# Kernel optimization log

Measured on AMD Instinct MI355X. Metric: run time of the kernel, lower is better.

The kernel has to match this reference:

```python
import jax, jax.numpy as jnp
import numpy as np

NUM_FIELDS = 39
VOCAB_PER_FIELD = 1000
EMB = 64
HEADS = 2
LAYERS = 3
BATCH = 16384
FLAT = NUM_FIELDS * EMB  # 2496


def _mhsa(x, Wq, Wk, Wv, Wr):
    # x: [B, n, D]; no scaling (scaling=False in source)
    B, n, D = x.shape
    dh = D // HEADS
    q = (x @ Wq).reshape(B, n, HEADS, dh)
    k = (x @ Wk).reshape(B, n, HEADS, dh)
    v = (x @ Wv).reshape(B, n, HEADS, dh)
    scores = jnp.einsum('bihd,bjhd->bhij', q, k)
    attn = jax.nn.softmax(scores, axis=-1)
    out = jnp.einsum('bhij,bjhd->bihd', attn, v).reshape(B, n, D)
    out = out + x @ Wr  # residual projection (use_res=True)
    return jax.nn.relu(out)


def setup_inputs() -> dict:
    key = jax.random.key(0)
    ks = jax.random.split(key, 12)
    X = jax.random.randint(ks[0], (BATCH, NUM_FIELDS), 0, VOCAB_PER_FIELD, dtype=jnp.int64 if jax.config.jax_enable_x64 else jnp.int32)
    emb_table = jax.random.normal(ks[1], (NUM_FIELDS * VOCAB_PER_FIELD, EMB), jnp.float32) * 0.05
    WQ = jax.random.normal(ks[2], (LAYERS, EMB, EMB), jnp.float32) * 0.05
    WK = jax.random.normal(ks[3], (LAYERS, EMB, EMB), jnp.float32) * 0.05
    WV = jax.random.normal(ks[4], (LAYERS, EMB, EMB), jnp.float32) * 0.05
    WR = jax.random.normal(ks[5], (LAYERS, EMB, EMB), jnp.float32) * 0.05
    W1 = jax.random.normal(ks[6], (FLAT, 512), jnp.float32) * 0.02
    b1 = jnp.zeros((512,), jnp.float32)
    W2 = jax.random.normal(ks[7], (512, 256), jnp.float32) * 0.02
    b2 = jnp.zeros((256,), jnp.float32)
    W3 = jax.random.normal(ks[8], (256, 1), jnp.float32) * 0.02
    b3 = jnp.zeros((1,), jnp.float32)
    Wlin = jax.random.normal(ks[9], (FLAT, 1), jnp.float32) * 0.02
    return {"X": X, "emb_table": emb_table, "WQ": WQ, "WK": WK, "WV": WV,
            "WR": WR, "W1": W1, "b1": b1, "W2": W2, "b2": b2, "W3": W3,
            "b3": b3, "Wlin": Wlin}


def reference(X, emb_table, WQ, WK, WV, WR, W1, b1, W2, b2, W3, b3, Wlin):
    offsets = jnp.arange(NUM_FIELDS, dtype=X.dtype) * VOCAB_PER_FIELD
    embed_x = emb_table[X + offsets[None, :]]  # [B, n, D]
    att = embed_x
    for i in range(LAYERS):
        att = _mhsa(att, WQ[i], WK[i], WV[i], WR[i])
    B = att.shape[0]
    att_output = jax.nn.relu(att.reshape(B, FLAT) @ Wlin)  # [B,1]
    # MLP: relu follows every Dense, including final 1-unit layer; dropout inactive
    h = embed_x.reshape(B, FLAT)
    h = jax.nn.relu(h @ W1 + b1)
    h = jax.nn.relu(h @ W2 + b2)
    dnn_output = jax.nn.relu(h @ W3 + b3)  # [B,1]
    return jax.nn.sigmoid(att_output + dnn_output)
```

## Files before the change

### kernel.cpp

```cpp
#include <hip/hip_runtime.h>
#include <hip/hip_bf16.h>


#define NF     39
#define EMB    64
#define NLAYER 3
#define VOCAB  1000
#define FLAT   2496
#define H1     512
#define H2     256

typedef __attribute__((ext_vector_type(8))) short  short8;
typedef __attribute__((ext_vector_type(4))) float  floatx4;

__device__ __forceinline__ short8 ld8s(const unsigned short* p) {
    return *(const short8*)p;
}
__device__ __forceinline__ float b2f(unsigned short h) {
    union { unsigned u; float f; } x; x.u = ((unsigned)h) << 16; return x.f;
}
__device__ __forceinline__ unsigned short f2b(float f) {
    union { float f; unsigned u; } x; x.f = f;
    unsigned u = x.u;
    return (unsigned short)((u + 0x7fffu + ((u >> 16) & 1u)) >> 16);
}
__device__ __forceinline__ unsigned cvt_pk(float a, float b) {
#if defined(__gfx950__)
    unsigned r;
    asm("v_cvt_pk_bf16_f32 %0, %1, %2" : "=v"(r) : "v"(a), "v"(b));
    return r;
#else
    return (unsigned)f2b(a) | ((unsigned)f2b(b) << 16);
#endif
}
__device__ __forceinline__ short8 pk8(unsigned a, unsigned b, unsigned c, unsigned d) {
    union { unsigned u[4]; short8 s; } x;
    x.u[0] = a; x.u[1] = b; x.u[2] = c; x.u[3] = d;
    return x.s;
}

__global__ void attw_t(const float* __restrict__ WQ, const float* __restrict__ WK,
                       const float* __restrict__ WV, const float* __restrict__ WR,
                       unsigned short* __restrict__ wqt, unsigned short* __restrict__ wkt,
                       unsigned short* __restrict__ wvt, unsigned short* __restrict__ wrt)
{
    int idx = blockIdx.x * 256 + threadIdx.x;
    if (idx >= 4 * 3 * 4096) return;
    int mat = idx / 12288;
    int rem = idx % 12288;
    int l   = rem / 4096;
    int ok  = rem % 4096;
    int o = ok >> 6, k = ok & 63;
    const float*    src = (mat == 0) ? WQ : (mat == 1) ? WK : (mat == 2) ? WV : WR;
    unsigned short* dst = (mat == 0) ? wqt : (mat == 1) ? wkt : (mat == 2) ? wvt : wrt;
    dst[l * 4096 + o * 64 + k] = f2b(src[l * 4096 + k * 64 + o]);
}

__global__ void w1pack(const float* __restrict__ W1, unsigned short* __restrict__ w1p)
{
    int t = blockIdx.x * 256 + threadIdx.x;
    int lane = t & 63, grp = t >> 6;
    int ot = grp / 78, kk = grp % 78;
    int q = lane >> 4, n = ot * 16 + (lane & 15);
    int kb = kk * 32 + q * 8;
    unsigned short* dst = w1p + grp * 512 + lane * 8;
    #pragma unroll
    for (int j = 0; j < 8; ++j)
        dst[j] = f2b(W1[(kb + j) * 512 + n]);
}

__global__ void w2pack(const float* __restrict__ W2, unsigned short* __restrict__ w2p)
{
    int t = blockIdx.x * 256 + threadIdx.x;
    int lane = t & 63, grp = t >> 6;
    int ot = grp / 16, kk = grp % 16;
    int q = lane >> 4, n = ot * 16 + (lane & 15);
    int kb = kk * 32 + q * 8;
    unsigned short* dst = w2p + grp * 512 + lane * 8;
    #pragma unroll
    for (int j = 0; j < 8; ++j)
        dst[j] = f2b(W2[(kb + j) * 256 + n]);
}

__global__ void __launch_bounds__(128) attn_kernel(
    const int* __restrict__ X,
    const float* __restrict__ embf,
    const unsigned short* __restrict__ wqt,
    const unsigned short* __restrict__ wkt,
    const unsigned short* __restrict__ wvt,
    const unsigned short* __restrict__ wrt,
    const float* __restrict__ wlinf,
    float* __restrict__ att_out)
{
    __shared__ unsigned short xss[48 * 72];
    __shared__ float red[2];

    const int tid  = threadIdx.x;
    const int wid  = tid >> 6;
    const int lane = tid & 63;
    const int h    = wid;
    const int quad = lane >> 4;
    const int l16  = lane & 15;
    const int samp = blockIdx.x;

    {
        const int tq = lane >> 4;
        const int cp = (lane & 15) * 2;
        const int col = h * 32 + cp;
        const int* xrow = X + samp * NF;
        #pragma unroll
        for (int t0 = 0; t0 < 48; t0 += 4) {
            int t = t0 + tq;
            unsigned pk = 0;
            if (t < NF) {
                int row = xrow[t] + t * VOCAB;
                const float2 v = *(const float2*)&embf[row * EMB + col];
                pk = cvt_pk(v.x, v.y);
            }
            *(unsigned*)&xss[t * 72 + col] = pk;
        }
    }
    __syncthreads();

    const int wro = (h * 32 + l16) * 64 + quad * 8;
    const unsigned short* wqp = wqt + wro;
    const unsigned short* wkp = wkt + wro;
    const unsigned short* wvq = wvt + wro;
    const unsigned short* wrp = wrt + wro;
    float m2[4];
    #pragma unroll
    for (int r = 0; r < 4; ++r)
        m2[r] = (32 + quad * 4 + r < NF) ? 1.f : 0.f;

    for (int layer = 0; layer < NLAYER; ++layer) {
        short8 xf[3][2];
        #pragma unroll
        for (int tt = 0; tt < 3; ++tt)
            #pragma unroll
            for (int kk = 0; kk < 2; ++kk)
                xf[tt][kk] = ld8s(&xss[(tt * 16 + l16) * 72 + kk * 32 + quad * 8]);

        __syncthreads();

        unsigned qw[2][3][2], kw[2][3][2];
        #pragma unroll
        for (int mat = 0; mat < 2; ++mat) {
            const unsigned short* wt = mat ? wkp : wqp;
            #pragma unroll
            for (int ot = 0; ot < 2; ++ot) {
                short8 w0 = ld8s(wt + ot * 1024);
                short8 w1 = ld8s(wt + ot * 1024 + 32);
                #pragma unroll
                for (int tt = 0; tt < 3; ++tt) {
                    floatx4 c = {0.f, 0.f, 0.f, 0.f};
                    c = __builtin_amdgcn_mfma_f32_16x16x32_bf16(w0, xf[tt][0], c, 0, 0, 0);
                    c = __builtin_amdgcn_mfma_f32_16x16x32_bf16(w1, xf[tt][1], c, 0, 0, 0);
                    if (mat == 0) {
                        qw[ot][tt][0] = cvt_pk(c[0], c[1]);
                        qw[ot][tt][1] = cvt_pk(c[2], c[3]);
                    } else {
                        kw[ot][tt][0] = cvt_pk(c[0], c[1]);
                        kw[ot][tt][1] = cvt_pk(c[2], c[3]);
                    }
                }
            }
        }

        floatx4 O[2][3];
        #pragma unroll
        for (int dt = 0; dt < 2; ++dt) {
            short8 w0 = ld8s(wrp + dt * 1024);
            short8 w1 = ld8s(wrp + dt * 1024 + 32);
            #pragma unroll
            for (int it = 0; it < 3; ++it) {
                floatx4 c = {0.f, 0.f, 0.f, 0.f};
                c = __builtin_amdgcn_mfma_f32_16x16x32_bf16(w0, xf[it][0], c, 0, 0, 0);
                c = __builtin_amdgcn_mfma_f32_16x16x32_bf16(w1, xf[it][1], c, 0, 0, 0);
                O[dt][it] = c;
            }
        }

        floatx4 ST[3][3];
        #pragma unroll
        for (int jt = 0; jt < 3; ++jt) {
            short8 a = pk8(kw[0][jt][0], kw[0][jt][1], kw[1][jt][0], kw[1][jt][1]);
            #pragma unroll
            for (int it = 0; it < 3; ++it) {
                short8 b = pk8(qw[0][it][0], qw[0][it][1], qw[1][it][0], qw[1][it][1]);
                floatx4 z = {0.f, 0.f, 0.f, 0.f};
                ST[jt][it] = __builtin_amdgcn_mfma_f32_16x16x32_bf16(a, b, z, 0, 0, 0);
            }
        }

        unsigned vw[3][2][2];
        #pragma unroll
        for (int nt = 0; nt < 2; ++nt) {
            short8 w0 = ld8s(wvq + nt * 1024);
            short8 w1 = ld8s(wvq + nt * 1024 + 32);
            #pragma unroll
            for (int mt = 0; mt < 3; ++mt) {
                floatx4 c = {0.f, 0.f, 0.f, 0.f};
                c = __builtin_amdgcn_mfma_f32_16x16x32_bf16(xf[mt][0], w0, c, 0, 0, 0);
                c = __builtin_amdgcn_mfma_f32_16x16x32_bf16(xf[mt][1], w1, c, 0, 0, 0);
                vw[mt][nt][0] = cvt_pk(c[0], c[1]);
                vw[mt][nt][1] = cvt_pk(c[2], c[3]);
            }
        }

        unsigned pw[3][3][2];
        #pragma unroll
        for (int it = 0; it < 3; ++it) {
            float p[3][4];
            float sum = 0.f;
            #pragma unroll
            for (int jt = 0; jt < 3; ++jt)
                #pragma unroll
                for (int r = 0; r < 4; ++r) {
                    float e = __expf(ST[jt][it][r]);
                    if (jt == 2) e *= m2[r];
                    p[jt][r] = e;
                    sum += e;
                }
            sum += __shfl_xor(sum, 16, 64);
            sum += __shfl_xor(sum, 32, 64);
            float inv = 1.0f / sum;
            #pragma unroll
            for (int jt = 0; jt < 3; ++jt) {
                pw[jt][it][0] = cvt_pk(p[jt][0] * inv, p[jt][1] * inv);
                pw[jt][it][1] = cvt_pk(p[jt][2] * inv, p[jt][3] * inv);
            }
        }

        #pragma unroll
        for (int dt = 0; dt < 2; ++dt) {
            short8 a01 = pk8(vw[0][dt][0], vw[0][dt][1], vw[1][dt][0], vw[1][dt][1]);
            short8 a2  = pk8(vw[2][dt][0], vw[2][dt][1], 0u, 0u);
            #pragma unroll
            for (int it = 0; it < 3; ++it) {
                short8 b01 = pk8(pw[0][it][0], pw[0][it][1], pw[1][it][0], pw[1][it][1]);
                short8 b2  = pk8(pw[2][it][0], pw[2][it][1], 0u, 0u);
                O[dt][it] = __builtin_amdgcn_mfma_f32_16x16x32_bf16(a01, b01, O[dt][it], 0, 0, 0);
                O[dt][it] = __builtin_amdgcn_mfma_f32_16x16x32_bf16(a2,  b2,  O[dt][it], 0, 0, 0);
            }
        }

        #pragma unroll
        for (int dt = 0; dt < 2; ++dt)
            #pragma unroll
            for (int it = 0; it < 3; ++it) {
                uint2 w;
                w.x = cvt_pk(fmaxf(O[dt][it][0], 0.f), fmaxf(O[dt][it][1], 0.f));
                w.y = cvt_pk(fmaxf(O[dt][it][2], 0.f), fmaxf(O[dt][it][3], 0.f));
                *(uint2*)&xss[(it * 16 + l16) * 72 + h * 32 + dt * 16 + quad * 4] = w;
            }

        __syncthreads();

        wqp += 4096; wkp += 4096; wvq += 4096; wrp += 4096;
    }

    {
        float acc = 0.f;
        const int c = lane & 31, tp = lane >> 5;
        const int col = h * 32 + c;
        for (int t0 = 0; t0 < 40; t0 += 2) {
            int t = t0 + tp;
            if (t < NF)
                acc += b2f(xss[t * 72 + col]) * wlinf[t * EMB + col];
        }
        #pragma unroll
        for (int off = 1; off < 64; off <<= 1)
            acc += __shfl_xor(acc, off, 64);
        if (lane == 0) red[wid] = acc;
        __syncthreads();
        if (tid == 0)
            att_out[samp] = fmaxf(red[0] + red[1], 0.f);
    }
}

__global__ void __launch_bounds__(256) dnn_kernel(
    const int* __restrict__ X,
    const float* __restrict__ embf,
    const unsigned short* __restrict__ w1p,
    const float* __restrict__ b1v,
    const unsigned short* __restrict__ w2p,
    const float* __restrict__ b2v,
    const float* __restrict__ w3v,
    const float* __restrict__ b3v,
    const float* __restrict__ att_in,
    float* __restrict__ out)
{
    __shared__ unsigned short ea[2][32 * 72];
    __shared__ unsigned short h1s[32 * 520];
    unsigned short* h2s = h1s;

    const int tid  = threadIdx.x;
    const int wid  = tid >> 6, lane = tid & 63, quad = lane >> 4, l16 = lane & 15;
    const int S0   = blockIdx.x * 32;

    floatx4 C1[2][8];
    #pragma unroll
    for (int mt = 0; mt < 2; ++mt)
        #pragma unroll
        for (int nt = 0; nt < 8; ++nt)
            C1[mt][nt] = (floatx4){0.f, 0.f, 0.f, 0.f};

    const int gs = tid >> 3;
    const int gg = tid & 7;

    {
        int row = X[(S0 + gs) * NF + 0];
        const float4* src = (const float4*)&embf[row * EMB + gg * 8];
        float4 v0 = src[0], v1 = src[1];
        uint4 u;
        u.x = cvt_pk(v0.x, v0.y); u.y = cvt_pk(v0.z, v0.w);
        u.z = cvt_pk(v1.x, v1.y); u.w = cvt_pk(v1.z, v1.w);
        *(uint4*)&ea[0][gs * 72 + gg * 8] = u;
    }
    __syncthreads();

    for (int f = 0; f < NF; ++f) {
        if (f < NF - 1) {
            int row = X[(S0 + gs) * NF + f + 1] + (f + 1) * VOCAB;
            const float4* src = (const float4*)&embf[row * EMB + gg * 8];
            float4 v0 = src[0], v1 = src[1];
            uint4 u;
            u.x = cvt_pk(v0.x, v0.y); u.y = cvt_pk(v0.z, v0.w);
            u.z = cvt_pk(v1.x, v1.y); u.w = cvt_pk(v1.z, v1.w);
            *(uint4*)&ea[(f + 1) & 1][gs * 72 + gg * 8] = u;
        }
        const unsigned short* eac = ea[f & 1];
        short8 a[2][2];
        #pragma unroll
        for (int mt = 0; mt < 2; ++mt) {
            a[mt][0] = ld8s(&eac[(mt * 16 + l16) * 72 + quad * 8]);
            a[mt][1] = ld8s(&eac[(mt * 16 + l16) * 72 + 32 + quad * 8]);
        }
        #pragma unroll
        for (int nt = 0; nt < 8; ++nt) {
            const unsigned short* bp = w1p + (((wid * 8 + nt) * 78 + f * 2) * 64 + lane) * 8;
            short8 b0 = ld8s(bp);
            short8 b1 = ld8s(bp + 512);
            #pragma unroll
            for (int mt = 0; mt < 2; ++mt) {
                C1[mt][nt] = __builtin_amdgcn_mfma_f32_16x16x32_bf16(a[mt][0], b0, C1[mt][nt], 0, 0, 0);
                C1[mt][nt] = __builtin_amdgcn_mfma_f32_16x16x32_bf16(a[mt][1], b1, C1[mt][nt], 0, 0, 0);
            }
        }
        __syncthreads();
    }

    #pragma unroll
    for (int nt = 0; nt < 8; ++nt) {
        float bb = b1v[wid * 128 + nt * 16 + l16];
        #pragma unroll
        for (int mt = 0; mt < 2; ++mt) {
            #pragma unroll
            for (int r = 0; r < 4; ++r) {
                float v = fmaxf(C1[mt][nt][r] + bb, 0.f);
                h1s[(mt * 16 + quad * 4 + r) * 520 + wid * 128 + nt * 16 + l16] = f2b(v);
            }
        }
    }
    __syncthreads();

    floatx4 C2[2][4];
    #pragma unroll
    for (int mt = 0; mt < 2; ++mt)
        #pragma unroll
        for (int nt = 0; nt < 4; ++nt)
            C2[mt][nt] = (floatx4){0.f, 0.f, 0.f, 0.f};

    #pragma unroll 4
    for (int kk = 0; kk < 16; ++kk) {
        short8 a0 = ld8s(&h1s[(l16) * 520 + kk * 32 + quad * 8]);
        short8 a1 = ld8s(&h1s[(16 + l16) * 520 + kk * 32 + quad * 8]);
        #pragma unroll
        for (int nt = 0; nt < 4; ++nt) {
            short8 b = ld8s(w2p + (((wid * 4 + nt) * 16 + kk) * 64 + lane) * 8);
            C2[0][nt] = __builtin_amdgcn_mfma_f32_16x16x32_bf16(a0, b, C2[0][nt], 0, 0, 0);
            C2[1][nt] = __builtin_amdgcn_mfma_f32_16x16x32_bf16(a1, b, C2[1][nt], 0, 0, 0);
        }
    }
    __syncthreads();

    #pragma unroll
    for (int nt = 0; nt < 4; ++nt) {
        float bb = b2v[wid * 64 + nt * 16 + l16];
        #pragma unroll
        for (int mt = 0; mt < 2; ++mt)
            #pragma unroll
            for (int r = 0; r < 4; ++r)
                h2s[(mt * 16 + quad * 4 + r) * 264 + wid * 64 + nt * 16 + l16] =
                    f2b(fmaxf(C2[mt][nt][r] + bb, 0.f));
    }
    __syncthreads();

    {
        int s = tid >> 3, part = tid & 7;
        float acc = 0.f;
        #pragma unroll 8
        for (int j = 0; j < 32; ++j) {
            int jj = part * 32 + j;
            acc += b2f(h2s[s * 264 + jj]) * w3v[jj];
        }
        acc += __shfl_xor(acc, 1, 64);
        acc += __shfl_xor(acc, 2, 64);
        acc += __shfl_xor(acc, 4, 64);
        if (part == 0) {
            float dnn = fmaxf(acc + b3v[0], 0.f);
            float v = dnn + att_in[S0 + s];
            out[S0 + s] = 1.f / (1.f + __expf(-v));
        }
    }
}

extern "C" void kernel_launch(void* const* d_in, const int* in_sizes, int n_in,
                              void* d_out, int out_size, void* d_ws, size_t ws_size,
                              hipStream_t stream)
{
    (void)in_sizes; (void)n_in; (void)out_size; (void)ws_size;

    const int*   X    = (const int*)d_in[0];
    const float* emb  = (const float*)d_in[1];
    const float* WQ   = (const float*)d_in[2];
    const float* WK   = (const float*)d_in[3];
    const float* WV   = (const float*)d_in[4];
    const float* WR   = (const float*)d_in[5];
    const float* W1   = (const float*)d_in[6];
    const float* b1   = (const float*)d_in[7];
    const float* W2   = (const float*)d_in[8];
    const float* b2   = (const float*)d_in[9];
    const float* W3   = (const float*)d_in[10];
    const float* b3   = (const float*)d_in[11];
    const float* Wlin = (const float*)d_in[12];

    char* ws = (char*)d_ws;
    float*          att_logit = (float*)ws;
    unsigned short* wqt = (unsigned short*)(ws + 65536);
    unsigned short* wkt = wqt + 3 * 4096;
    unsigned short* wvt = wkt + 3 * 4096;
    unsigned short* wrt = wvt + 3 * 4096;
    unsigned short* w1p = wrt + 3 * 4096;
    unsigned short* w2p = w1p + 2496 * 512;

    attw_t<<<192, 256, 0, stream>>>(WQ, WK, WV, WR, wqt, wkt, wvt, wrt);
    w1pack<<<624, 256, 0, stream>>>(W1, w1p);
    w2pack<<<64, 256, 0, stream>>>(W2, w2p);
    attn_kernel<<<16384, 128, 0, stream>>>(X, emb, wqt, wkt, wvt, wrt, Wlin, att_logit);
    dnn_kernel<<<512, 256, 0, stream>>>(X, emb, w1p, b1, w2p, b2, W3, b3, att_logit,
                                        (float*)d_out);
}
```

Baseline: 378.4 us.

## Process two samples per attention block to reuse weight fragments

The attention kernel now handles two samples per 128-thread block, halving the grid. Each Q/K/V/R weight fragment loaded from global memory is reused across both samples' MFMAs, and block launch and barrier overhead is amortized over two samples. In exchange, register pressure roughly doubles (two sets of Q/K/V/O fragments) and shared memory doubles, which could reduce occupancy or cause spills.

```diff
diff --git a/kernel.cpp b/kernel.cpp
--- a/kernel.cpp
+++ b/kernel.cpp
@@ -92,8 +92,8 @@
     const float* __restrict__ wlinf,
     float* __restrict__ att_out)
 {
-    __shared__ unsigned short xss[48 * 72];
-    __shared__ float red[2];
+    __shared__ unsigned short xss[2][48 * 72];
+    __shared__ float red[2][2];
 
     const int tid  = threadIdx.x;
     const int wid  = tid >> 6;
@@ -101,23 +101,26 @@
     const int h    = wid;
     const int quad = lane >> 4;
     const int l16  = lane & 15;
-    const int samp = blockIdx.x;
+    const int samp0 = blockIdx.x * 2;
 
     {
         const int tq = lane >> 4;
         const int cp = (lane & 15) * 2;
         const int col = h * 32 + cp;
-        const int* xrow = X + samp * NF;
-        #pragma unroll
-        for (int t0 = 0; t0 < 48; t0 += 4) {
-            int t = t0 + tq;
-            unsigned pk = 0;
-            if (t < NF) {
-                int row = xrow[t] + t * VOCAB;
-                const float2 v = *(const float2*)&embf[row * EMB + col];
-                pk = cvt_pk(v.x, v.y);
-            }
-            *(unsigned*)&xss[t * 72 + col] = pk;
+        #pragma unroll
+        for (int s = 0; s < 2; ++s) {
+            const int* xrow = X + (samp0 + s) * NF;
+            #pragma unroll
+            for (int t0 = 0; t0 < 48; t0 += 4) {
+                int t = t0 + tq;
+                unsigned pk = 0;
+                if (t < NF) {
+                    int row = xrow[t] + t * VOCAB;
+                    const float2 v = *(const float2*)&embf[row * EMB + col];
+                    pk = cvt_pk(v.x, v.y);
+                }
+                *(unsigned*)&xss[s][t * 72 + col] = pk;
+            }
         }
     }
     __syncthreads();
@@ -133,16 +136,18 @@
         m2[r] = (32 + quad * 4 + r < NF) ? 1.f : 0.f;
 
     for (int layer = 0; layer < NLAYER; ++layer) {
-        short8 xf[3][2];
-        #pragma unroll
-        for (int tt = 0; tt < 3; ++tt)
-            #pragma unroll
-            for (int kk = 0; kk < 2; ++kk)
-                xf[tt][kk] = ld8s(&xss[(tt * 16 + l16) * 72 + kk * 32 + quad * 8]);
+        short8 xf[2][3][2];
+        #pragma unroll
+        for (int s = 0; s < 2; ++s)
+            #pragma unroll
+            for (int tt = 0; tt < 3; ++tt)
+                #pragma unroll
+                for (int kk = 0; kk < 2; ++kk)
+                    xf[s][tt][kk] = ld8s(&xss[s][(tt * 16 + l16) * 72 + kk * 32 + quad * 8]);
 
         __syncthreads();
 
-        unsigned qw[2][3][2], kw[2][3][2];
+        unsigned qw[2][2][3][2], kw[2][2][3][2];
         #pragma unroll
         for (int mat = 0; mat < 2; ++mat) {
             const unsigned short* wt = mat ? wkp : wqp;
@@ -151,108 +156,120 @@
                 short8 w0 = ld8s(wt + ot * 1024);
                 short8 w1 = ld8s(wt + ot * 1024 + 32);
                 #pragma unroll
-                for (int tt = 0; tt < 3; ++tt) {
-                    floatx4 c = {0.f, 0.f, 0.f, 0.f};
-                    c = __builtin_amdgcn_mfma_f32_16x16x32_bf16(w0, xf[tt][0], c, 0, 0, 0);
-                    c = __builtin_amdgcn_mfma_f32_16x16x32_bf16(w1, xf[tt][1], c, 0, 0, 0);
-                    if (mat == 0) {
-                        qw[ot][tt][0] = cvt_pk(c[0], c[1]);
-                        qw[ot][tt][1] = cvt_pk(c[2], c[3]);
-                    } else {
-                        kw[ot][tt][0] = cvt_pk(c[0], c[1]);
-                        kw[ot][tt][1] = cvt_pk(c[2], c[3]);
+                for (int s = 0; s < 2; ++s)
+                    #pragma unroll
+                    for (int tt = 0; tt < 3; ++tt) {
+                        floatx4 c = {0.f, 0.f, 0.f, 0.f};
+                        c = __builtin_amdgcn_mfma_f32_16x16x32_bf16(w0, xf[s][tt][0], c, 0, 0, 0);
+                        c = __builtin_amdgcn_mfma_f32_16x16x32_bf16(w1, xf[s][tt][1], c, 0, 0, 0);
+                        if (mat == 0) {
+                            qw[s][ot][tt][0] = cvt_pk(c[0], c[1]);
+                            qw[s][ot][tt][1] = cvt_pk(c[2], c[3]);
+                        } else {
+                            kw[s][ot][tt][0] = cvt_pk(c[0], c[1]);
+                            kw[s][ot][tt][1] = cvt_pk(c[2], c[3]);
+                        }
                     }
-                }
-            }
-        }
-
-        floatx4 O[2][3];
+            }
+        }
+
+        floatx4 O[2][2][3];
         #pragma unroll
         for (int dt = 0; dt < 2; ++dt) {
             short8 w0 = ld8s(wrp + dt * 1024);
             short8 w1 = ld8s(wrp + dt * 1024 + 32);
             #pragma unroll
-            for (int it = 0; it < 3; ++it) {
-                floatx4 c = {0.f, 0.f, 0.f, 0.f};
-                c = __builtin_amdgcn_mfma_f32_16x16x32_bf16(w0, xf[it][0], c, 0, 0, 0);
-                c = __builtin_amdgcn_mfma_f32_16x16x32_bf16(w1, xf[it][1], c, 0, 0, 0);
-                O[dt][it] = c;
-            }
-        }
-
-        floatx4 ST[3][3];
-        #pragma unroll
-        for (int jt = 0; jt < 3; ++jt) {
-            short8 a = pk8(kw[0][jt][0], kw[0][jt][1], kw[1][jt][0], kw[1][jt][1]);
-            #pragma unroll
-            for (int it = 0; it < 3; ++it) {
-                short8 b = pk8(qw[0][it][0], qw[0][it][1], qw[1][it][0], qw[1][it][1]);
-                floatx4 z = {0.f, 0.f, 0.f, 0.f};
-                ST[jt][it] = __builtin_amdgcn_mfma_f32_16x16x32_bf16(a, b, z, 0, 0, 0);
-            }
-        }
-
-        unsigned vw[3][2][2];
+            for (int s = 0; s < 2; ++s)
+                #pragma unroll
+                for (int it = 0; it < 3; ++it) {
+                    floatx4 c = {0.f, 0.f, 0.f, 0.f};
+                    c = __builtin_amdgcn_mfma_f32_16x16x32_bf16(w0, xf[s][it][0], c, 0, 0, 0);
+                    c = __builtin_amdgcn_mfma_f32_16x16x32_bf16(w1, xf[s][it][1], c, 0, 0, 0);
+                    O[s][dt][it] = c;
+                }
+        }
+
+        unsigned vw[2][3][2][2];
         #pragma unroll
         for (int nt = 0; nt < 2; ++nt) {
             short8 w0 = ld8s(wvq + nt * 1024);
             short8 w1 = ld8s(wvq + nt * 1024 + 32);
             #pragma unroll
-            for (int mt = 0; mt < 3; ++mt) {
-                floatx4 c = {0.f, 0.f, 0.f, 0.f};
-                c = __builtin_amdgcn_mfma_f32_16x16x32_bf16(xf[mt][0], w0, c, 0, 0, 0);
-                c = __builtin_amdgcn_mfma_f32_16x16x32_bf16(xf[mt][1], w1, c, 0, 0, 0);
-                vw[mt][nt][0] = cvt_pk(c[0], c[1]);
-                vw[mt][nt][1] = cvt_pk(c[2], c[3]);
-            }
-        }
-
-        unsigned pw[3][3][2];
-        #pragma unroll
-        for (int it = 0; it < 3; ++it) {
-            float p[3][4];
-            float sum = 0.f;
-            #pragma unroll
-            for (int jt = 0; jt < 3; ++jt)
-                #pragma unroll
-                for (int r = 0; r < 4; ++r) {
-                    float e = __expf(ST[jt][it][r]);
-                    if (jt == 2) e *= m2[r];
-                    p[jt][r] = e;
-                    sum += e;
-                }
-            sum += __shfl_xor(sum, 16, 64);
-            sum += __shfl_xor(sum, 32, 64);
-            float inv = 1.0f / sum;
+            for (int s = 0; s < 2; ++s)
+                #pragma unroll
+                for (int mt = 0; mt < 3; ++mt) {
+                    floatx4 c = {0.f, 0.f, 0.f, 0.f};
+                    c = __builtin_amdgcn_mfma_f32_16x16x32_bf16(xf[s][mt][0], w0, c, 0, 0, 0);
+                    c = __builtin_amdgcn_mfma_f32_16x16x32_bf16(xf[s][mt][1], w1, c, 0, 0, 0);
+                    vw[s][mt][nt][0] = cvt_pk(c[0], c[1]);
+                    vw[s][mt][nt][1] = cvt_pk(c[2], c[3]);
+                }
+        }
+
+        unsigned pw[2][3][3][2];
+        #pragma unroll
+        for (int s = 0; s < 2; ++s) {
+            floatx4 ST[3][3];
             #pragma unroll
             for (int jt = 0; jt < 3; ++jt) {
-                pw[jt][it][0] = cvt_pk(p[jt][0] * inv, p[jt][1] * inv);
-                pw[jt][it][1] = cvt_pk(p[jt][2] * inv, p[jt][3] * inv);
-            }
-        }
-
-        #pragma unroll
-        for (int dt = 0; dt < 2; ++dt) {
-            short8 a01 = pk8(vw[0][dt][0], vw[0][dt][1], vw[1][dt][0], vw[1][dt][1]);
-            short8 a2  = pk8(vw[2][dt][0], vw[2][dt][1], 0u, 0u);
+                short8 a = pk8(kw[s][0][jt][0], kw[s][0][jt][1], kw[s][1][jt][0], kw[s][1][jt][1]);
+                #pragma unroll
+                for (int it = 0; it < 3; ++it) {
+                    short8 b = pk8(qw[s][0][it][0], qw[s][0][it][1], qw[s][1][it][0], qw[s][1][it][1]);
+                    floatx4 z = {0.f, 0.f, 0.f, 0.f};
+                    ST[jt][it] = __builtin_amdgcn_mfma_f32_16x16x32_bf16(a, b, z, 0, 0, 0);
+                }
+            }
             #pragma unroll
             for (int it = 0; it < 3; ++it) {
-                short8 b01 = pk8(pw[0][it][0], pw[0][it][1], pw[1][it][0], pw[1][it][1]);
-                short8 b2  = pk8(pw[2][it][0], pw[2][it][1], 0u, 0u);
-                O[dt][it] = __builtin_amdgcn_mfma_f32_16x16x32_bf16(a01, b01, O[dt][it], 0, 0, 0);
-                O[dt][it] = __builtin_amdgcn_mfma_f32_16x16x32_bf16(a2,  b2,  O[dt][it], 0, 0, 0);
-            }
-        }
-
-        #pragma unroll
-        for (int dt = 0; dt < 2; ++dt)
-            #pragma unroll
-            for (int it = 0; it < 3; ++it) {
-                uint2 w;
-                w.x = cvt_pk(fmaxf(O[dt][it][0], 0.f), fmaxf(O[dt][it][1], 0.f));
-                w.y = cvt_pk(fmaxf(O[dt][it][2], 0.f), fmaxf(O[dt][it][3], 0.f));
-                *(uint2*)&xss[(it * 16 + l16) * 72 + h * 32 + dt * 16 + quad * 4] = w;
-            }
+                float p[3][4];
+                float sum = 0.f;
+                #pragma unroll
+                for (int jt = 0; jt < 3; ++jt)
+                    #pragma unroll
+                    for (int r = 0; r < 4; ++r) {
+                        float e = __expf(ST[jt][it][r]);
+                        if (jt == 2) e *= m2[r];
+                        p[jt][r] = e;
+                        sum += e;
+                    }
+                sum += __shfl_xor(sum, 16, 64);
+                sum += __shfl_xor(sum, 32, 64);
+                float inv = 1.0f / sum;
+                #pragma unroll
+                for (int jt = 0; jt < 3; ++jt) {
+                    pw[s][jt][it][0] = cvt_pk(p[jt][0] * inv, p[jt][1] * inv);
+                    pw[s][jt][it][1] = cvt_pk(p[jt][2] * inv, p[jt][3] * inv);
+                }
+            }
+        }
+
+        #pragma unroll
+        for (int s = 0; s < 2; ++s)
+            #pragma unroll
+            for (int dt = 0; dt < 2; ++dt) {
+                short8 a01 = pk8(vw[s][0][dt][0], vw[s][0][dt][1], vw[s][1][dt][0], vw[s][1][dt][1]);
+                short8 a2  = pk8(vw[s][2][dt][0], vw[s][2][dt][1], 0u, 0u);
+                #pragma unroll
+                for (int it = 0; it < 3; ++it) {
+                    short8 b01 = pk8(pw[s][0][it][0], pw[s][0][it][1], pw[s][1][it][0], pw[s][1][it][1]);
+                    short8 b2  = pk8(pw[s][2][it][0], pw[s][2][it][1], 0u, 0u);
+                    O[s][dt][it] = __builtin_amdgcn_mfma_f32_16x16x32_bf16(a01, b01, O[s][dt][it], 0, 0, 0);
+                    O[s][dt][it] = __builtin_amdgcn_mfma_f32_16x16x32_bf16(a2,  b2,  O[s][dt][it], 0, 0, 0);
+                }
+            }
+
+        #pragma unroll
+        for (int s = 0; s < 2; ++s)
+            #pragma unroll
+            for (int dt = 0; dt < 2; ++dt)
+                #pragma unroll
+                for (int it = 0; it < 3; ++it) {
+                    uint2 w;
+                    w.x = cvt_pk(fmaxf(O[s][dt][it][0], 0.f), fmaxf(O[s][dt][it][1], 0.f));
+                    w.y = cvt_pk(fmaxf(O[s][dt][it][2], 0.f), fmaxf(O[s][dt][it][3], 0.f));
+                    *(uint2*)&xss[s][(it * 16 + l16) * 72 + h * 32 + dt * 16 + quad * 4] = w;
+                }
 
         __syncthreads();
 
@@ -260,21 +277,26 @@
     }
 
     {
-        float acc = 0.f;
         const int c = lane & 31, tp = lane >> 5;
         const int col = h * 32 + c;
-        for (int t0 = 0; t0 < 40; t0 += 2) {
-            int t = t0 + tp;
-            if (t < NF)
-                acc += b2f(xss[t * 72 + col]) * wlinf[t * EMB + col];
-        }
-        #pragma unroll
-        for (int off = 1; off < 64; off <<= 1)
-            acc += __shfl_xor(acc, off, 64);
-        if (lane == 0) red[wid] = acc;
+        #pragma unroll
+        for (int s = 0; s < 2; ++s) {
+            float acc = 0.f;
+            for (int t0 = 0; t0 < 40; t0 += 2) {
+                int t = t0 + tp;
+                if (t < NF)
+                    acc += b2f(xss[s][t * 72 + col]) * wlinf[t * EMB + col];
+            }
+            #pragma unroll
+            for (int off = 1; off < 64; off <<= 1)
+                acc += __shfl_xor(acc, off, 64);
+            if (lane == 0) red[s][wid] = acc;
+        }
         __syncthreads();
-        if (tid == 0)
-            att_out[samp] = fmaxf(red[0] + red[1], 0.f);
+        if (tid == 0) {
+            att_out[samp0]     = fmaxf(red[0][0] + red[0][1], 0.f);
+            att_out[samp0 + 1] = fmaxf(red[1][0] + red[1][1], 0.f);
+        }
     }
 }
 
@@ -447,7 +469,7 @@
     attw_t<<<192, 256, 0, stream>>>(WQ, WK, WV, WR, wqt, wkt, wvt, wrt);
     w1pack<<<624, 256, 0, stream>>>(W1, w1p);
     w2pack<<<64, 256, 0, stream>>>(W2, w2p);
-    attn_kernel<<<16384, 128, 0, stream>>>(X, emb, wqt, wkt, wvt, wrt, Wlin, att_logit);
+    attn_kernel<<<8192, 128, 0, stream>>>(X, emb, wqt, wkt, wvt, wrt, Wlin, att_logit);
     dnn_kernel<<<512, 256, 0, stream>>>(X, emb, w1p, b1, w2p, b2, W3, b3, att_logit,
                                         (float*)d_out);
 }
```

Measured after the change: 362.8 us. 1.04x faster.

## Run one sample per wavefront with register-resident activations, dropping LDS round trips

Applied to the files above, without the earlier changes.

The attention kernel now gives each wavefront a whole sample covering both heads, with four samples per 256-thread block, instead of two wavefronts per sample, one per head. Activations stay in registers between layers as packed bf16 MFMA operands. To make this work, the weight transpose permutes the K index so the MFMA output layout matches the next layer's input layout. This removes shared-memory staging, block barriers and the cross-wave reduction, but raises register pressure and doubles per-wave MFMA work.

```diff
diff --git a/kernel.cpp b/kernel.cpp
--- a/kernel.cpp
+++ b/kernel.cpp
@@ -19,6 +19,8 @@
 __device__ __forceinline__ float b2f(unsigned short h) {
     union { unsigned u; float f; } x; x.u = ((unsigned)h) << 16; return x.f;
 }
+__device__ __forceinline__ float b2f_lo(unsigned w) { return b2f((unsigned short)(w & 0xffffu)); }
+__device__ __forceinline__ float b2f_hi(unsigned w) { return b2f((unsigned short)(w >> 16)); }
 __device__ __forceinline__ unsigned short f2b(float f) {
     union { float f; unsigned u; } x; x.f = f;
     unsigned u = x.u;
@@ -50,10 +52,12 @@
     int rem = idx % 12288;
     int l   = rem / 4096;
     int ok  = rem % 4096;
-    int o = ok >> 6, k = ok & 63;
+    int o = ok >> 6, pos = ok & 63;
+    int kk = pos >> 5, q = (pos >> 3) & 3, e = pos & 7;
+    int k = kk * 32 + (e >> 2) * 16 + q * 4 + (e & 3);
     const float*    src = (mat == 0) ? WQ : (mat == 1) ? WK : (mat == 2) ? WV : WR;
     unsigned short* dst = (mat == 0) ? wqt : (mat == 1) ? wkt : (mat == 2) ? wvt : wrt;
-    dst[l * 4096 + o * 64 + k] = f2b(src[l * 4096 + k * 64 + o]);
+    dst[l * 4096 + o * 64 + pos] = f2b(src[l * 4096 + k * 64 + o]);
 }
 
 __global__ void w1pack(const float* __restrict__ W1, unsigned short* __restrict__ w1p)
@@ -82,7 +86,7 @@
         dst[j] = f2b(W2[(kb + j) * 256 + n]);
 }
 
-__global__ void __launch_bounds__(128) attn_kernel(
+__global__ void __launch_bounds__(256) attn_kernel(
     const int* __restrict__ X,
     const float* __restrict__ embf,
     const unsigned short* __restrict__ wqt,
@@ -92,190 +96,199 @@
     const float* __restrict__ wlinf,
     float* __restrict__ att_out)
 {
-    __shared__ unsigned short xss[48 * 72];
-    __shared__ float red[2];
-
     const int tid  = threadIdx.x;
     const int wid  = tid >> 6;
     const int lane = tid & 63;
-    const int h    = wid;
     const int quad = lane >> 4;
     const int l16  = lane & 15;
-    const int samp = blockIdx.x;
-
+    const int samp = blockIdx.x * 4 + wid;
+
+    unsigned xiw[3][2][4];
     {
-        const int tq = lane >> 4;
-        const int cp = (lane & 15) * 2;
-        const int col = h * 32 + cp;
         const int* xrow = X + samp * NF;
         #pragma unroll
-        for (int t0 = 0; t0 < 48; t0 += 4) {
-            int t = t0 + tq;
-            unsigned pk = 0;
-            if (t < NF) {
-                int row = xrow[t] + t * VOCAB;
-                const float2 v = *(const float2*)&embf[row * EMB + col];
-                pk = cvt_pk(v.x, v.y);
-            }
-            *(unsigned*)&xss[t * 72 + col] = pk;
-        }
-    }
-    __syncthreads();
-
-    const int wro = (h * 32 + l16) * 64 + quad * 8;
-    const unsigned short* wqp = wqt + wro;
-    const unsigned short* wkp = wkt + wro;
-    const unsigned short* wvq = wvt + wro;
-    const unsigned short* wrp = wrt + wro;
+        for (int tt = 0; tt < 3; ++tt) {
+            const int tok = tt * 16 + l16;
+            if (tok < NF) {
+                const int row = xrow[tok] + tok * VOCAB;
+                const float* er = embf + row * EMB;
+                #pragma unroll
+                for (int kk = 0; kk < 2; ++kk) {
+                    const float4 lo = *(const float4*)(er + kk * 32 + quad * 4);
+                    const float4 hi = *(const float4*)(er + kk * 32 + 16 + quad * 4);
+                    xiw[tt][kk][0] = cvt_pk(lo.x, lo.y);
+                    xiw[tt][kk][1] = cvt_pk(lo.z, lo.w);
+                    xiw[tt][kk][2] = cvt_pk(hi.x, hi.y);
+                    xiw[tt][kk][3] = cvt_pk(hi.z, hi.w);
+                }
+            } else {
+                #pragma unroll
+                for (int kk = 0; kk < 2; ++kk)
+                    #pragma unroll
+                    for (int w = 0; w < 4; ++w)
+                        xiw[tt][kk][w] = 0u;
+            }
+        }
+    }
+
+    const int wro_l = l16 * 64 + quad * 8;
+    const unsigned short* wq = wqt + wro_l;
+    const unsigned short* wk = wkt + wro_l;
+    const unsigned short* wv = wvt + wro_l;
+    const unsigned short* wr = wrt + wro_l;
     float m2[4];
     #pragma unroll
     for (int r = 0; r < 4; ++r)
         m2[r] = (32 + quad * 4 + r < NF) ? 1.f : 0.f;
 
+    #define XF(tt,kk) pk8(xiw[tt][kk][0], xiw[tt][kk][1], xiw[tt][kk][2], xiw[tt][kk][3])
+
     for (int layer = 0; layer < NLAYER; ++layer) {
-        short8 xf[3][2];
-        #pragma unroll
-        for (int tt = 0; tt < 3; ++tt)
-            #pragma unroll
-            for (int kk = 0; kk < 2; ++kk)
-                xf[tt][kk] = ld8s(&xss[(tt * 16 + l16) * 72 + kk * 32 + quad * 8]);
-
-        __syncthreads();
-
-        unsigned qw[2][3][2], kw[2][3][2];
-        #pragma unroll
-        for (int mat = 0; mat < 2; ++mat) {
-            const unsigned short* wt = mat ? wkp : wqp;
-            #pragma unroll
-            for (int ot = 0; ot < 2; ++ot) {
-                short8 w0 = ld8s(wt + ot * 1024);
-                short8 w1 = ld8s(wt + ot * 1024 + 32);
-                #pragma unroll
-                for (int tt = 0; tt < 3; ++tt) {
-                    floatx4 c = {0.f, 0.f, 0.f, 0.f};
-                    c = __builtin_amdgcn_mfma_f32_16x16x32_bf16(w0, xf[tt][0], c, 0, 0, 0);
-                    c = __builtin_amdgcn_mfma_f32_16x16x32_bf16(w1, xf[tt][1], c, 0, 0, 0);
-                    if (mat == 0) {
-                        qw[ot][tt][0] = cvt_pk(c[0], c[1]);
-                        qw[ot][tt][1] = cvt_pk(c[2], c[3]);
-                    } else {
-                        kw[ot][tt][0] = cvt_pk(c[0], c[1]);
-                        kw[ot][tt][1] = cvt_pk(c[2], c[3]);
+        unsigned pw[2][3][3][2];
+        #pragma unroll
+        for (int h = 0; h < 2; ++h) {
+            unsigned qw[2][3][2], kw[2][3][2];
+            #pragma unroll
+            for (int mat = 0; mat < 2; ++mat) {
+                const unsigned short* wt = (mat ? wk : wq) + h * 2048;
+                #pragma unroll
+                for (int ot = 0; ot < 2; ++ot) {
+                    short8 w0 = ld8s(wt + ot * 1024);
+                    short8 w1 = ld8s(wt + ot * 1024 + 32);
+                    #pragma unroll
+                    for (int tt = 0; tt < 3; ++tt) {
+                        floatx4 c = {0.f, 0.f, 0.f, 0.f};
+                        c = __builtin_amdgcn_mfma_f32_16x16x32_bf16(w0, XF(tt,0), c, 0, 0, 0);
+                        c = __builtin_amdgcn_mfma_f32_16x16x32_bf16(w1, XF(tt,1), c, 0, 0, 0);
+                        if (mat == 0) {
+                            qw[ot][tt][0] = cvt_pk(c[0], c[1]);
+                            qw[ot][tt][1] = cvt_pk(c[2], c[3]);
+                        } else {
+                            kw[ot][tt][0] = cvt_pk(c[0], c[1]);
+                            kw[ot][tt][1] = cvt_pk(c[2], c[3]);
+                        }
                     }
                 }
             }
-        }
-
-        floatx4 O[2][3];
-        #pragma unroll
-        for (int dt = 0; dt < 2; ++dt) {
-            short8 w0 = ld8s(wrp + dt * 1024);
-            short8 w1 = ld8s(wrp + dt * 1024 + 32);
+            floatx4 ST[3][3];
+            #pragma unroll
+            for (int jt = 0; jt < 3; ++jt) {
+                short8 a = pk8(kw[0][jt][0], kw[0][jt][1], kw[1][jt][0], kw[1][jt][1]);
+                #pragma unroll
+                for (int it = 0; it < 3; ++it) {
+                    short8 b = pk8(qw[0][it][0], qw[0][it][1], qw[1][it][0], qw[1][it][1]);
+                    floatx4 z = {0.f, 0.f, 0.f, 0.f};
+                    ST[jt][it] = __builtin_amdgcn_mfma_f32_16x16x32_bf16(a, b, z, 0, 0, 0);
+                }
+            }
+            #pragma unroll
+            for (int it = 0; it < 3; ++it) {
+                float p[3][4];
+                float sum = 0.f;
+                #pragma unroll
+                for (int jt = 0; jt < 3; ++jt)
+                    #pragma unroll
+                    for (int r = 0; r < 4; ++r) {
+                        float e = __expf(ST[jt][it][r]);
+                        if (jt == 2) e *= m2[r];
+                        p[jt][r] = e;
+                        sum += e;
+                    }
+                sum += __shfl_xor(sum, 16, 64);
+                sum += __shfl_xor(sum, 32, 64);
+                float inv = 1.0f / sum;
+                #pragma unroll
+                for (int jt = 0; jt < 3; ++jt) {
+                    pw[h][jt][it][0] = cvt_pk(p[jt][0] * inv, p[jt][1] * inv);
+                    pw[h][jt][it][1] = cvt_pk(p[jt][2] * inv, p[jt][3] * inv);
+                }
+            }
+        }
+
+        unsigned vw[3][4][2];
+        #pragma unroll
+        for (int nt = 0; nt < 4; ++nt) {
+            short8 w0 = ld8s(wv + nt * 1024);
+            short8 w1 = ld8s(wv + nt * 1024 + 32);
+            #pragma unroll
+            for (int mt = 0; mt < 3; ++mt) {
+                floatx4 c = {0.f, 0.f, 0.f, 0.f};
+                c = __builtin_amdgcn_mfma_f32_16x16x32_bf16(XF(mt,0), w0, c, 0, 0, 0);
+                c = __builtin_amdgcn_mfma_f32_16x16x32_bf16(XF(mt,1), w1, c, 0, 0, 0);
+                vw[mt][nt][0] = cvt_pk(c[0], c[1]);
+                vw[mt][nt][1] = cvt_pk(c[2], c[3]);
+            }
+        }
+
+        floatx4 O[4][3];
+        #pragma unroll
+        for (int dt = 0; dt < 4; ++dt) {
+            short8 w0 = ld8s(wr + dt * 1024);
+            short8 w1 = ld8s(wr + dt * 1024 + 32);
             #pragma unroll
             for (int it = 0; it < 3; ++it) {
                 floatx4 c = {0.f, 0.f, 0.f, 0.f};
-                c = __builtin_amdgcn_mfma_f32_16x16x32_bf16(w0, xf[it][0], c, 0, 0, 0);
-                c = __builtin_amdgcn_mfma_f32_16x16x32_bf16(w1, xf[it][1], c, 0, 0, 0);
+                c = __builtin_amdgcn_mfma_f32_16x16x32_bf16(w0, XF(it,0), c, 0, 0, 0);
+                c = __builtin_amdgcn_mfma_f32_16x16x32_bf16(w1, XF(it,1), c, 0, 0, 0);
                 O[dt][it] = c;
             }
         }
 
-        floatx4 ST[3][3];
-        #pragma unroll
-        for (int jt = 0; jt < 3; ++jt) {
-            short8 a = pk8(kw[0][jt][0], kw[0][jt][1], kw[1][jt][0], kw[1][jt][1]);
-            #pragma unroll
-            for (int it = 0; it < 3; ++it) {
-                short8 b = pk8(qw[0][it][0], qw[0][it][1], qw[1][it][0], qw[1][it][1]);
-                floatx4 z = {0.f, 0.f, 0.f, 0.f};
-                ST[jt][it] = __builtin_amdgcn_mfma_f32_16x16x32_bf16(a, b, z, 0, 0, 0);
-            }
-        }
-
-        unsigned vw[3][2][2];
-        #pragma unroll
-        for (int nt = 0; nt < 2; ++nt) {
-            short8 w0 = ld8s(wvq + nt * 1024);
-            short8 w1 = ld8s(wvq + nt * 1024 + 32);
-            #pragma unroll
-            for (int mt = 0; mt < 3; ++mt) {
-                floatx4 c = {0.f, 0.f, 0.f, 0.f};
-                c = __builtin_amdgcn_mfma_f32_16x16x32_bf16(xf[mt][0], w0, c, 0, 0, 0);
-                c = __builtin_amdgcn_mfma_f32_16x16x32_bf16(xf[mt][1], w1, c, 0, 0, 0);
-                vw[mt][nt][0] = cvt_pk(c[0], c[1]);
-                vw[mt][nt][1] = cvt_pk(c[2], c[3]);
-            }
-        }
-
-        unsigned pw[3][3][2];
-        #pragma unroll
-        for (int it = 0; it < 3; ++it) {
-            float p[3][4];
-            float sum = 0.f;
-            #pragma unroll
-            for (int jt = 0; jt < 3; ++jt)
-                #pragma unroll
-                for (int r = 0; r < 4; ++r) {
-                    float e = __expf(ST[jt][it][r]);
-                    if (jt == 2) e *= m2[r];
-                    p[jt][r] = e;
-                    sum += e;
-                }
-            sum += __shfl_xor(sum, 16, 64);
-            sum += __shfl_xor(sum, 32, 64);
-            float inv = 1.0f / sum;
-            #pragma unroll
-            for (int jt = 0; jt < 3; ++jt) {
-                pw[jt][it][0] = cvt_pk(p[jt][0] * inv, p[jt][1] * inv);
-                pw[jt][it][1] = cvt_pk(p[jt][2] * inv, p[jt][3] * inv);
-            }
-        }
-
-        #pragma unroll
-        for (int dt = 0; dt < 2; ++dt) {
-            short8 a01 = pk8(vw[0][dt][0], vw[0][dt][1], vw[1][dt][0], vw[1][dt][1]);
-            short8 a2  = pk8(vw[2][dt][0], vw[2][dt][1], 0u, 0u);
-            #pragma unroll
-            for (int it = 0; it < 3; ++it) {
-                short8 b01 = pk8(pw[0][it][0], pw[0][it][1], pw[1][it][0], pw[1][it][1]);
-                short8 b2  = pk8(pw[2][it][0], pw[2][it][1], 0u, 0u);
-                O[dt][it] = __builtin_amdgcn_mfma_f32_16x16x32_bf16(a01, b01, O[dt][it], 0, 0, 0);
-                O[dt][it] = __builtin_amdgcn_mfma_f32_16x16x32_bf16(a2,  b2,  O[dt][it], 0, 0, 0);
-            }
-        }
-
-        #pragma unroll
-        for (int dt = 0; dt < 2; ++dt)
-            #pragma unroll
-            for (int it = 0; it < 3; ++it) {
-                uint2 w;
-                w.x = cvt_pk(fmaxf(O[dt][it][0], 0.f), fmaxf(O[dt][it][1], 0.f));
-                w.y = cvt_pk(fmaxf(O[dt][it][2], 0.f), fmaxf(O[dt][it][3], 0.f));
-                *(uint2*)&xss[(it * 16 + l16) * 72 + h * 32 + dt * 16 + quad * 4] = w;
-            }
-
-        __syncthreads();
-
-        wqp += 4096; wkp += 4096; wvq += 4096; wrp += 4096;
+        #pragma unroll
+        for (int h = 0; h < 2; ++h)
+            #pragma unroll
+            for (int dtl = 0; dtl < 2; ++dtl) {
+                const int dt = h * 2 + dtl;
+                short8 a01 = pk8(vw[0][dt][0], vw[0][dt][1], vw[1][dt][0], vw[1][dt][1]);
+                short8 a2  = pk8(vw[2][dt][0], vw[2][dt][1], 0u, 0u);
+                #pragma unroll
+                for (int it = 0; it < 3; ++it) {
+                    short8 b01 = pk8(pw[h][0][it][0], pw[h][0][it][1], pw[h][1][it][0], pw[h][1][it][1]);
+                    short8 b2  = pk8(pw[h][2][it][0], pw[h][2][it][1], 0u, 0u);
+                    O[dt][it] = __builtin_amdgcn_mfma_f32_16x16x32_bf16(a01, b01, O[dt][it], 0, 0, 0);
+                    O[dt][it] = __builtin_amdgcn_mfma_f32_16x16x32_bf16(a2,  b2,  O[dt][it], 0, 0, 0);
+                }
+            }
+
+        #pragma unroll
+        for (int it = 0; it < 3; ++it)
+            #pragma unroll
+            for (int kk = 0; kk < 2; ++kk) {
+                const int d0 = kk * 2, d1 = kk * 2 + 1;
+                xiw[it][kk][0] = cvt_pk(fmaxf(O[d0][it][0], 0.f), fmaxf(O[d0][it][1], 0.f));
+                xiw[it][kk][1] = cvt_pk(fmaxf(O[d0][it][2], 0.f), fmaxf(O[d0][it][3], 0.f));
+                xiw[it][kk][2] = cvt_pk(fmaxf(O[d1][it][0], 0.f), fmaxf(O[d1][it][1], 0.f));
+                xiw[it][kk][3] = cvt_pk(fmaxf(O[d1][it][2], 0.f), fmaxf(O[d1][it][3], 0.f));
+            }
+
+        wq += 4096; wk += 4096; wv += 4096; wr += 4096;
     }
 
     {
         float acc = 0.f;
-        const int c = lane & 31, tp = lane >> 5;
-        const int col = h * 32 + c;
-        for (int t0 = 0; t0 < 40; t0 += 2) {
-            int t = t0 + tp;
-            if (t < NF)
-                acc += b2f(xss[t * 72 + col]) * wlinf[t * EMB + col];
+        #pragma unroll
+        for (int tt = 0; tt < 3; ++tt) {
+            const int tok = tt * 16 + l16;
+            if (tok < NF) {
+                const float* wl = wlinf + tok * EMB;
+                #pragma unroll
+                for (int kk = 0; kk < 2; ++kk) {
+                    const float4 A = *(const float4*)(wl + kk * 32 + quad * 4);
+                    const float4 B = *(const float4*)(wl + kk * 32 + 16 + quad * 4);
+                    acc += b2f_lo(xiw[tt][kk][0]) * A.x + b2f_hi(xiw[tt][kk][0]) * A.y;
+                    acc += b2f_lo(xiw[tt][kk][1]) * A.z + b2f_hi(xiw[tt][kk][1]) * A.w;
+                    acc += b2f_lo(xiw[tt][kk][2]) * B.x + b2f_hi(xiw[tt][kk][2]) * B.y;
+                    acc += b2f_lo(xiw[tt][kk][3]) * B.z + b2f_hi(xiw[tt][kk][3]) * B.w;
+                }
+            }
         }
         #pragma unroll
         for (int off = 1; off < 64; off <<= 1)
             acc += __shfl_xor(acc, off, 64);
-        if (lane == 0) red[wid] = acc;
-        __syncthreads();
-        if (tid == 0)
-            att_out[samp] = fmaxf(red[0] + red[1], 0.f);
-    }
+        if (lane == 0)
+            att_out[samp] = fmaxf(acc, 0.f);
+    }
+    #undef XF
 }
 
 __global__ void __launch_bounds__(256) dnn_kernel(
@@ -447,7 +460,7 @@
     attw_t<<<192, 256, 0, stream>>>(WQ, WK, WV, WR, wqt, wkt, wvt, wrt);
     w1pack<<<624, 256, 0, stream>>>(W1, w1p);
     w2pack<<<64, 256, 0, stream>>>(W2, w2p);
-    attn_kernel<<<16384, 128, 0, stream>>>(X, emb, wqt, wkt, wvt, wrt, Wlin, att_logit);
+    attn_kernel<<<4096, 256, 0, stream>>>(X, emb, wqt, wkt, wvt, wrt, Wlin, att_logit);
     dnn_kernel<<<512, 256, 0, stream>>>(X, emb, w1p, b1, w2p, b2, W3, b3, att_logit,
                                         (float*)d_out);
 }
```

New measurement: 404.2 us. 1.07x slower.
